# Optimization experiments

Hardware: AMD Instinct MI355X
Metric: run time of the kernel (lower is better)

The kernel has to match this reference:

```python
import jax, jax.numpy as jnp
import numpy as np

N, M = 1024, 32
FN, FE = 64, 32
AGG_N, AGG_E = 128, 64
OUT_N, OUT_E = 64, 32


def _build_indices(n, m):
    nip, eip = [], []
    k = 0
    for i in range(1, n):
        j0 = max(0, i - m)
        nip += list(range(j0, i))
        eip += list(range(k, k + i - j0))
        k += i - j0
    n1 = np.array(nip, np.int32)
    eT = np.array(eip, np.int32)
    n2 = np.concatenate([np.full(min(i, m), i, np.int32) for i in range(1, n)])
    # padded previous-node window indices (0 = zero pad slot)
    prev_nodes = np.zeros(n * m, np.int32)
    k = 0
    for i in range(n):
        t = min(i, m)
        prev_nodes[(i + 1) * m - t:(i + 1) * m] = np.arange(k, k + t) + 1
        k += t
    n_e = k
    norm_node = np.full(n, 1.0 / m, np.float32)
    for i in range(1, m):
        norm_node[i] = 1.0 / i
    prev_edges = np.zeros(n_e * m, np.int32)
    k = 0
    e = 0
    for i in range(n):
        j0 = max(0, i - m)
        for j in range(j0, i):
            if j > j0:
                prev_edges[(e + 1) * m - (j - j0):(e + 1) * m] = np.arange(k, k + j - j0) + 1
            e += 1
        k += i - j0
    norm_edge = np.ones(n_e, np.float32)
    k = 0
    for i in range(1, n):
        t = min(i, m)
        for j in range(t):
            if j > 0:
                norm_edge[k] = 1.0 / j
            k += 1
    return n1, eT, n2, prev_nodes, norm_node, prev_edges, norm_edge, n_e

N1, ET, N2, PREV_N, NORM_N, PREV_E, NORM_E, NE = _build_indices(N, M)
N1 = jnp.asarray(N1); ET = jnp.asarray(ET); N2 = jnp.asarray(N2)
PREV_N = jnp.asarray(PREV_N); PREV_E = jnp.asarray(PREV_E)
NORM_N = jnp.asarray(NORM_N); NORM_E = jnp.asarray(NORM_E)


def setup_inputs() -> dict:
    key = jax.random.key(0)
    ks = jax.random.split(key, 20)
    s = 0.02
    inp = {
        'input_nodes': jax.random.normal(ks[0], (2, N, FN), jnp.float32),
        'input_edges': jax.random.normal(ks[1], (2, NE, FE), jnp.float32),
        # node-branch MLPs (exclude_last=False)
        'Wan1': jax.random.normal(ks[2], (2 * FN + FE, 2 * AGG_N)) * s,
        'ban1': jnp.zeros((2 * AGG_N,)),
        'Wan2': jax.random.normal(ks[3], (2 * AGG_N, AGG_N)) * s,
        'ban2': jnp.zeros((AGG_N,)),
        'Wln1': jax.random.normal(ks[4], (AGG_N + FN, AGG_N + FN)) * s,
        'bln1': jnp.zeros((AGG_N + FN,)),
        'Wln2': jax.random.normal(ks[5], (AGG_N + FN, OUT_N)) * s,
        'bln2': jnp.zeros((OUT_N,)),
        # edge-branch MLPs
        'Wae1': jax.random.normal(ks[6], (FN + FE, 2 * AGG_E)) * s,
        'bae1': jnp.zeros((2 * AGG_E,)),
        'Wae2': jax.random.normal(ks[7], (2 * AGG_E, AGG_E)) * s,
        'bae2': jnp.zeros((AGG_E,)),
        'Wle1': jax.random.normal(ks[8], (AGG_E + FE, AGG_E + FE)) * s,
        'ble1': jnp.zeros((AGG_E + FE,)),
        'Wle2': jax.random.normal(ks[9], (AGG_E + FE, OUT_E)) * s,
        'ble2': jnp.zeros((OUT_E,)),
    }
    return inp


def _mlp2(x, W1, b1, W2, b2):
    return jax.nn.relu(jax.nn.relu(x @ W1 + b1) @ W2 + b2)


def reference(input_nodes, input_edges, Wan1, ban1, Wan2, ban2, Wln1, bln1, Wln2, bln2,
              Wae1, bae1, Wae2, bae2, Wle1, ble1, Wle2, ble2):
    B = input_nodes.shape[0]
    # gather node-edge pairs [B, NE, FN+FE] and node-edge-node triples [B, NE, 2FN+FE]
    pairs = jnp.concatenate([input_nodes[:, N1], input_edges[:, ET]], axis=-1)
    triples = jnp.concatenate([input_nodes[:, N1], input_edges[:, ET], input_nodes[:, N2]], axis=-1)
    # node branch (exclude_last=False -> triples)
    hn = _mlp2(triples, Wan1, ban1, Wan2, ban2)                     # [B, NE, AGG_N]
    hn = jnp.concatenate([jnp.zeros((B, 1, AGG_N), hn.dtype), hn], axis=1)
    pn = hn[:, PREV_N].reshape(B, N, M, AGG_N).sum(axis=2)          # padded window sum
    pn = pn * NORM_N[None, :, None]
    nodes_in = jnp.concatenate([pn, input_nodes], axis=-1)
    out_nodes = _mlp2(nodes_in, Wln1, bln1, Wln2, bln2)             # activation_nodes = relu
    # edge branch (pairs)
    he = _mlp2(pairs, Wae1, bae1, Wae2, bae2)                       # [B, NE, AGG_E]
    he = jnp.concatenate([jnp.zeros((B, 1, AGG_E), he.dtype), he], axis=1)
    pe = he[:, PREV_E].reshape(B, NE, M, AGG_E).sum(axis=2)
    pe = pe * NORM_E[None, :, None]
    edges_in = jnp.concatenate([pe, input_edges], axis=-1)
    out_edges = _mlp2(edges_in, Wle1, ble1, Wle2, ble2)             # activation_edges = relu
    return out_nodes, out_edges
```

## Files before the change

### kernel.cpp

```cpp
#include <hip/hip_runtime.h>
#include <cstdint>

#define NN    1024
#define MM    32
#define NEDGE 32240
#define MROWS 64480
#define PX    168
#define PSTN  264
#define PXE   104
#define PH1   136
#define PHE   72
#define EHALF 9984

typedef unsigned short ushort_t;

typedef __bf16 bf16x8 __attribute__((ext_vector_type(8)));
typedef float  floatx4 __attribute__((ext_vector_type(4)));

__device__ __forceinline__ float b2f(ushort_t u) {
    union { unsigned int i; float f; } v; v.i = ((unsigned int)u) << 16; return v.f;
}
__device__ __forceinline__ ushort_t f2b(float f) {
    return __builtin_bit_cast(ushort_t, (__bf16)f);
}
__device__ __forceinline__ int edge_base(int i) {
    return (i <= MM) ? ((i * (i - 1)) >> 1) : (496 + (i - MM) * MM);
}

__global__ __launch_bounds__(256) void k_pack(
        const float* an1, const float* an2, const float* ae1, const float* ae2,
        const float* le1, const float* le2, const float* ln1, const float* ln2,
        const float* nodes, const float* edges,
        ushort_t* pan1, ushort_t* pan2, ushort_t* pae1, ushort_t* pae2,
        ushort_t* ple1, ushort_t* ple2, ushort_t* pln1, ushort_t* pln2,
        ushort_t* nodesb, ushort_t* edgesb) {
    __shared__ float tile[32][33];
    const int bid = blockIdx.x;
    const int tid = threadIdx.x;
    if (bid < 152) {
        const float* s; ushort_t* d; int K, N, t;
        if (bid < 40)       { s = an1; d = pan1; K = 160; N = 256; t = bid;       }
        else if (bid < 72)  { s = an2; d = pan2; K = 256; N = 128; t = bid - 40;  }
        else if (bid < 84)  { s = ae1; d = pae1; K = 96;  N = 128; t = bid - 72;  }
        else if (bid < 92)  { s = ae2; d = pae2; K = 128; N = 64;  t = bid - 84;  }
        else if (bid < 101) { s = le1; d = ple1; K = 96;  N = 96;  t = bid - 92;  }
        else if (bid < 104) { s = le2; d = ple2; K = 96;  N = 32;  t = bid - 101; }
        else if (bid < 140) { s = ln1; d = pln1; K = 192; N = 192; t = bid - 104; }
        else                { s = ln2; d = pln2; K = 192; N = 64;  t = bid - 140; }
        int ntn = N >> 5;
        int tk = t / ntn, tn = t - tk * ntn;
        int k0 = tk * 32, n0 = tn * 32;
        int tx = tid & 31, ty = tid >> 5;
#pragma unroll
        for (int m = 0; m < 4; ++m)
            tile[ty + m * 8][tx] = s[(size_t)(k0 + ty + m * 8) * N + n0 + tx];
        __syncthreads();
#pragma unroll
        for (int m = 0; m < 4; ++m)
            d[(size_t)(n0 + ty + m * 8) * K + k0 + tx] = f2b(tile[tx][ty + m * 8]);
    } else if (bid < 280) {
        int i4 = (bid - 152) * 256 + tid;
        float4 v = ((const float4*)nodes)[i4];
        uint2 o;
        o.x = (unsigned)f2b(v.x) | ((unsigned)f2b(v.y) << 16);
        o.y = (unsigned)f2b(v.z) | ((unsigned)f2b(v.w) << 16);
        ((uint2*)nodesb)[i4] = o;
    } else {
        int i4 = (bid - 280) * 256 + tid;
        if (i4 < 515840) {
            float4 v = ((const float4*)edges)[i4];
            uint2 o;
            o.x = (unsigned)f2b(v.x) | ((unsigned)f2b(v.y) << 16);
            o.y = (unsigned)f2b(v.z) | ((unsigned)f2b(v.w) << 16);
            ((uint2*)edgesb)[i4] = o;
        }
    }
}

__global__ __launch_bounds__(512, 4) void k_main(
        const ushort_t* __restrict__ nodesb, const ushort_t* __restrict__ edgesb,
        const ushort_t* __restrict__ pan1, const float* __restrict__ ban1,
        const ushort_t* __restrict__ pan2, const float* __restrict__ ban2,
        const ushort_t* __restrict__ pae1, const float* __restrict__ bae1,
        const ushort_t* __restrict__ pae2, const float* __restrict__ bae2,
        const ushort_t* __restrict__ ple1, const float* __restrict__ ble1,
        const ushort_t* __restrict__ ple2, const float* __restrict__ ble2,
        ushort_t* __restrict__ pn, float* __restrict__ out_edges) {
    __shared__ alignas(16) ushort_t SH[2 * EHALF];
    const int tid = threadIdx.x;
    const int w = tid >> 6, l = tid & 63, lrow = l & 15, lq = l >> 4;
    const int bid = blockIdx.x;
    floatx4 zero = {0.f, 0.f, 0.f, 0.f};

    if (bid < 2048) {
        const int b = bid >> 10, i = bid & 1023;
        const int t = min(i, MM);
        if (i == 0) {
            if (tid < 64) ((unsigned*)(pn + (size_t)bid * 128))[tid] = 0u;
            return;
        }
        const int j0 = i - t;
        const int base = b * NEDGE + edge_base(i);
        ushort_t* X = SH;
        ushort_t* H = SH + 32 * PX;

        bf16x8 B0[5], B1[5];
#pragma unroll
        for (int kt = 0; kt < 5; ++kt) {
            B0[kt] = *(const bf16x8*)(pan1 + (size_t)(16 * w + lrow) * 160 + kt * 32 + lq * 8);
            B1[kt] = *(const bf16x8*)(pan1 + (size_t)(16 * (w + 8) + lrow) * 160 + kt * 32 + lq * 8);
        }
        float c0 = ban1[16 * w + lrow];
        float c1 = ban1[16 * (w + 8) + lrow];

#pragma unroll
        for (int k = 0; k < 4; ++k) {
            int rr = w * 4 + k;
            unsigned* xr = (unsigned*)(X + rr * PX);
            const unsigned* nj = (const unsigned*)(nodesb + (size_t)(b * NN + j0 + rr) * 64);
            const unsigned* ni = (const unsigned*)(nodesb + (size_t)(b * NN + i) * 64);
            const unsigned* eb = (const unsigned*)(edgesb + (size_t)(base + rr) * 32);
            if (l < 32) { xr[l] = nj[l]; xr[48 + l] = ni[l]; }
            else        xr[l] = eb[l - 32];
        }
        __syncthreads();

#pragma unroll
        for (int s = 0; s < 2; ++s) {
            bf16x8 A[5];
#pragma unroll
            for (int kt = 0; kt < 5; ++kt)
                A[kt] = *(const bf16x8*)&X[(s * 16 + lrow) * PX + kt * 32 + lq * 8];
            floatx4 a0 = zero, a1 = zero;
#pragma unroll
            for (int kt = 0; kt < 5; ++kt) {
                a0 = __builtin_amdgcn_mfma_f32_16x16x32_bf16(A[kt], B0[kt], a0, 0, 0, 0);
                a1 = __builtin_amdgcn_mfma_f32_16x16x32_bf16(A[kt], B1[kt], a1, 0, 0, 0);
            }
#pragma unroll
            for (int r_ = 0; r_ < 4; ++r_) {
                int row = (s * 16 + lq * 4 + r_) * PSTN;
                H[row + 16 * w + lrow]       = f2b(fmaxf(a0[r_] + c0, 0.f));
                H[row + 128 + 16 * w + lrow] = f2b(fmaxf(a1[r_] + c1, 0.f));
            }
        }
        __syncthreads();

        {
            bf16x8 D[8];
#pragma unroll
            for (int kt = 0; kt < 8; ++kt)
                D[kt] = *(const bf16x8*)(pan2 + (size_t)(16 * w + lrow) * 256 + kt * 32 + lq * 8);
            float d0 = ban2[16 * w + lrow];
            float P = 0.f;
#pragma unroll
            for (int s = 0; s < 2; ++s) {
                floatx4 a0 = zero;
#pragma unroll
                for (int kt = 0; kt < 8; ++kt) {
                    bf16x8 a = *(const bf16x8*)&H[(s * 16 + lrow) * PSTN + kt * 32 + lq * 8];
                    a0 = __builtin_amdgcn_mfma_f32_16x16x32_bf16(a, D[kt], a0, 0, 0, 0);
                }
#pragma unroll
                for (int r_ = 0; r_ < 4; ++r_) {
                    int row = s * 16 + lq * 4 + r_;
                    float v = fmaxf(a0[r_] + d0, 0.f);
                    float vr = b2f(f2b(v));
                    if (row < t) P += vr;
                }
            }
            P += __shfl_xor(P, 16);
            P += __shfl_xor(P, 32);
            if (l < 16)
                pn[(size_t)bid * 128 + 16 * w + lrow] = f2b(P * (1.0f / (float)t));
        }
    } else {
        const int q = bid - 2048;
        const int h = w >> 2, w4 = w & 3;
        const int lt = tid & 255;
        const int ri = 2 * q + h;
        const int b = ri >> 10, i = ri & 1023;
        const int t = min(i, MM);
        const int j0 = i - t;
        const int base = b * NEDGE + edge_base(i);
        ushort_t* Xe = SH + h * EHALF;
        ushort_t* H1 = Xe + 3328;
        ushort_t* HE = H1 + 4352;
        ushort_t* LB = H1;

        bf16x8 B0[3], B1[3];
#pragma unroll
        for (int kt = 0; kt < 3; ++kt) {
            B0[kt] = *(const bf16x8*)(pae1 + (size_t)(16 * w4 + lrow) * 96 + kt * 32 + lq * 8);
            B1[kt] = *(const bf16x8*)(pae1 + (size_t)(16 * (w4 + 4) + lrow) * 96 + kt * 32 + lq * 8);
        }
        const float c0 = bae1[16 * w4 + lrow];
        const float c1 = bae1[16 * (w4 + 4) + lrow];

        for (int u = lt; u < 32 * 48; u += 256) {
            int row = u / 48, c = u - row * 48;
            unsigned v;
            if (c < 32) v = ((const unsigned*)nodesb)[(size_t)(b * NN + j0 + row) * 32 + c];
            else        v = ((const unsigned*)edgesb)[(size_t)(base + row) * 16 + (c - 32)];
            ((unsigned*)Xe)[row * (PXE / 2) + c] = v;
        }
        __syncthreads();

#pragma unroll
        for (int s = 0; s < 2; ++s) {
            bf16x8 A[3];
#pragma unroll
            for (int kt = 0; kt < 3; ++kt)
                A[kt] = *(const bf16x8*)&Xe[(s * 16 + lrow) * PXE + kt * 32 + lq * 8];
            floatx4 a0 = zero, a1 = zero;
#pragma unroll
            for (int kt = 0; kt < 3; ++kt) {
                a0 = __builtin_amdgcn_mfma_f32_16x16x32_bf16(A[kt], B0[kt], a0, 0, 0, 0);
                a1 = __builtin_amdgcn_mfma_f32_16x16x32_bf16(A[kt], B1[kt], a1, 0, 0, 0);
            }
#pragma unroll
            for (int r_ = 0; r_ < 4; ++r_) {
                int row = (s * 16 + lq * 4 + r_) * PH1;
                H1[row + 16 * w4 + lrow]      = f2b(fmaxf(a0[r_] + c0, 0.f));
                H1[row + 64 + 16 * w4 + lrow] = f2b(fmaxf(a1[r_] + c1, 0.f));
            }
        }
        __syncthreads();

        {
            bf16x8 E[4];
#pragma unroll
            for (int kt = 0; kt < 4; ++kt)
                E[kt] = *(const bf16x8*)(pae2 + (size_t)(16 * w4 + lrow) * 128 + kt * 32 + lq * 8);
            float d2 = bae2[16 * w4 + lrow];
#pragma unroll
            for (int s = 0; s < 2; ++s) {
                floatx4 a2 = zero;
#pragma unroll
                for (int kt = 0; kt < 4; ++kt) {
                    bf16x8 a = *(const bf16x8*)&H1[(s * 16 + lrow) * PH1 + kt * 32 + lq * 8];
                    a2 = __builtin_amdgcn_mfma_f32_16x16x32_bf16(a, E[kt], a2, 0, 0, 0);
                }
#pragma unroll
                for (int r_ = 0; r_ < 4; ++r_)
                    HE[(s * 16 + lq * 4 + r_) * PHE + 16 * w4 + lrow] = f2b(fmaxf(a2[r_] + d2, 0.f));
            }
        }
        if (l < 16) {
            float run = 0.f;
            for (int p = 0; p < t; ++p) {
                Xe[p * PXE + 16 * w4 + l] = f2b((p == 0) ? 0.f : run / (float)p);
                run += b2f(HE[p * PHE + 16 * w4 + l]);
            }
        }
        __syncthreads();

        {
            bf16x8 F0[3], F1[3];
            const bool two = (w4 < 2);
#pragma unroll
            for (int kt = 0; kt < 3; ++kt) {
                F0[kt] = *(const bf16x8*)(ple1 + (size_t)(16 * w4 + lrow) * 96 + kt * 32 + lq * 8);
                if (two)
                    F1[kt] = *(const bf16x8*)(ple1 + (size_t)(16 * (w4 + 4) + lrow) * 96 + kt * 32 + lq * 8);
            }
            float v0 = ble1[16 * w4 + lrow];
            float v1 = two ? ble1[16 * (w4 + 4) + lrow] : 0.f;
#pragma unroll
            for (int s = 0; s < 2; ++s) {
                bf16x8 A[3];
#pragma unroll
                for (int kt = 0; kt < 3; ++kt)
                    A[kt] = *(const bf16x8*)&Xe[(s * 16 + lrow) * PXE + kt * 32 + lq * 8];
                floatx4 a0 = zero, a1 = zero;
#pragma unroll
                for (int kt = 0; kt < 3; ++kt) {
                    a0 = __builtin_amdgcn_mfma_f32_16x16x32_bf16(A[kt], F0[kt], a0, 0, 0, 0);
                    if (two)
                        a1 = __builtin_amdgcn_mfma_f32_16x16x32_bf16(A[kt], F1[kt], a1, 0, 0, 0);
                }
#pragma unroll
                for (int r_ = 0; r_ < 4; ++r_) {
                    int row = (s * 16 + lq * 4 + r_) * PXE;
                    LB[row + 16 * w4 + lrow] = f2b(fmaxf(a0[r_] + v0, 0.f));
                    if (two)
                        LB[row + 64 + 16 * w4 + lrow] = f2b(fmaxf(a1[r_] + v1, 0.f));
                }
            }
        }
        __syncthreads();

        {
            int ct = w4 & 1, s = w4 >> 1;
            int c0o = 16 * ct;
            bf16x8 F2[3];
#pragma unroll
            for (int kt = 0; kt < 3; ++kt)
                F2[kt] = *(const bf16x8*)(ple2 + (size_t)(c0o + lrow) * 96 + kt * 32 + lq * 8);
            float v2 = ble2[c0o + lrow];
            floatx4 a2 = zero;
#pragma unroll
            for (int kt = 0; kt < 3; ++kt) {
                bf16x8 a = *(const bf16x8*)&LB[(s * 16 + lrow) * PXE + kt * 32 + lq * 8];
                a2 = __builtin_amdgcn_mfma_f32_16x16x32_bf16(a, F2[kt], a2, 0, 0, 0);
            }
#pragma unroll
            for (int r_ = 0; r_ < 4; ++r_) {
                int grow = s * 16 + lq * 4 + r_;
                if (grow < t)
                    out_edges[(size_t)(base + grow) * 32 + c0o + lrow] = fmaxf(a2[r_] + v2, 0.f);
            }
        }
    }
}

__global__ __launch_bounds__(192) void k_final(
        const ushort_t* __restrict__ pn, const ushort_t* __restrict__ nodesb,
        const ushort_t* __restrict__ pln1, const float* __restrict__ bln1,
        const ushort_t* __restrict__ pln2, const float* __restrict__ bln2,
        float* __restrict__ out_nodes) {
    __shared__ alignas(16) ushort_t LA[32 * 200];
    __shared__ alignas(16) ushort_t LB[32 * 200];
    const int tid = threadIdx.x;
    const int w = tid >> 6, l = tid & 63, lrow = l & 15, lq = l >> 4;
    floatx4 zero = {0.f, 0.f, 0.f, 0.f};

    int tile = blockIdx.x;
    for (int u = tid; u < 768; u += 192) {
        int row = u / 24, c = u - row * 24;
        int r = tile * 32 + row;
        const uint4* src = (c < 16) ? ((const uint4*)(pn + (size_t)r * 128) + c)
                                    : ((const uint4*)(nodesb + (size_t)r * 64) + (c - 16));
        *(uint4*)&LA[row * 200 + c * 8] = *src;
    }
    bf16x8 f1[6][4]; float v1[4];
#pragma unroll
    for (int kt = 0; kt < 6; ++kt)
#pragma unroll
        for (int nt = 0; nt < 4; ++nt)
            f1[kt][nt] = *(const bf16x8*)(pln1 + (size_t)(w * 64 + nt * 16 + lrow) * 192 + kt * 32 + lq * 8);
#pragma unroll
    for (int nt = 0; nt < 4; ++nt) v1[nt] = bln1[w * 64 + nt * 16 + lrow];
    __syncthreads();

    floatx4 acc[2][4];
#pragma unroll
    for (int s = 0; s < 2; ++s)
#pragma unroll
        for (int nt = 0; nt < 4; ++nt) acc[s][nt] = zero;
#pragma unroll
    for (int s = 0; s < 2; ++s)
#pragma unroll
        for (int kt = 0; kt < 6; ++kt) {
            bf16x8 a = *(const bf16x8*)&LA[(s * 16 + lrow) * 200 + kt * 32 + lq * 8];
#pragma unroll
            for (int nt = 0; nt < 4; ++nt)
                acc[s][nt] = __builtin_amdgcn_mfma_f32_16x16x32_bf16(a, f1[kt][nt], acc[s][nt], 0, 0, 0);
        }
#pragma unroll
    for (int s = 0; s < 2; ++s)
#pragma unroll
        for (int nt = 0; nt < 4; ++nt) {
            int col = w * 64 + nt * 16 + lrow;
#pragma unroll
            for (int r_ = 0; r_ < 4; ++r_)
                LB[(s * 16 + lq * 4 + r_) * 200 + col] = f2b(fmaxf(acc[s][nt][r_] + v1[nt], 0.f));
        }
    bf16x8 f2[6][2]; float v2[2] = {0.f, 0.f};
    if (w < 2) {
#pragma unroll
        for (int kt = 0; kt < 6; ++kt)
#pragma unroll
            for (int nt = 0; nt < 2; ++nt)
                f2[kt][nt] = *(const bf16x8*)(pln2 + (size_t)(w * 32 + nt * 16 + lrow) * 192 + kt * 32 + lq * 8);
#pragma unroll
        for (int nt = 0; nt < 2; ++nt) v2[nt] = bln2[w * 32 + nt * 16 + lrow];
    }
    __syncthreads();
    if (w < 2) {
        floatx4 a2[2][2];
#pragma unroll
        for (int s = 0; s < 2; ++s) { a2[s][0] = zero; a2[s][1] = zero; }
#pragma unroll
        for (int s = 0; s < 2; ++s)
#pragma unroll
            for (int kt = 0; kt < 6; ++kt) {
                bf16x8 a = *(const bf16x8*)&LB[(s * 16 + lrow) * 200 + kt * 32 + lq * 8];
#pragma unroll
                for (int nt = 0; nt < 2; ++nt)
                    a2[s][nt] = __builtin_amdgcn_mfma_f32_16x16x32_bf16(a, f2[kt][nt], a2[s][nt], 0, 0, 0);
            }
#pragma unroll
        for (int s = 0; s < 2; ++s)
#pragma unroll
            for (int nt = 0; nt < 2; ++nt) {
                int col = w * 32 + nt * 16 + lrow;
#pragma unroll
                for (int r_ = 0; r_ < 4; ++r_)
                    out_nodes[(size_t)(tile * 32 + s * 16 + lq * 4 + r_) * 64 + col] =
                        fmaxf(a2[s][nt][r_] + v2[nt], 0.f);
            }
    }
}

extern "C" void kernel_launch(void* const* d_in, const int* in_sizes, int n_in,
                              void* d_out, int out_size, void* d_ws, size_t ws_size,
                              hipStream_t stream) {
    const float* nodes = (const float*)d_in[0];
    const float* edges = (const float*)d_in[1];
    const float* Wan1 = (const float*)d_in[2];  const float* ban1 = (const float*)d_in[3];
    const float* Wan2 = (const float*)d_in[4];  const float* ban2 = (const float*)d_in[5];
    const float* Wln1 = (const float*)d_in[6];  const float* bln1 = (const float*)d_in[7];
    const float* Wln2 = (const float*)d_in[8];  const float* bln2 = (const float*)d_in[9];
    const float* Wae1 = (const float*)d_in[10]; const float* bae1 = (const float*)d_in[11];
    const float* Wae2 = (const float*)d_in[12]; const float* bae2 = (const float*)d_in[13];
    const float* Wle1 = (const float*)d_in[14]; const float* ble1 = (const float*)d_in[15];
    const float* Wle2 = (const float*)d_in[16]; const float* ble2 = (const float*)d_in[17];

    char* ws = (char*)d_ws;
    size_t o = 0;
    auto alloc = [&](size_t bytes) -> void* {
        void* r = ws + o;
        o += (bytes + 255) & ~(size_t)255;
        return r;
    };
    ushort_t* pn     = (ushort_t*)alloc((size_t)2048 * 128 * 2);
    ushort_t* nodesb = (ushort_t*)alloc((size_t)2 * NN * 64 * 2);
    ushort_t* edgesb = (ushort_t*)alloc((size_t)MROWS * 32 * 2);
    ushort_t* pan1 = (ushort_t*)alloc(160 * 256 * 2);
    ushort_t* pan2 = (ushort_t*)alloc(256 * 128 * 2);
    ushort_t* pae1 = (ushort_t*)alloc(96 * 128 * 2);
    ushort_t* pae2 = (ushort_t*)alloc(128 * 64 * 2);
    ushort_t* ple1 = (ushort_t*)alloc(96 * 96 * 2);
    ushort_t* ple2 = (ushort_t*)alloc(96 * 32 * 2);
    ushort_t* pln1 = (ushort_t*)alloc(192 * 192 * 2);
    ushort_t* pln2 = (ushort_t*)alloc(192 * 64 * 2);

    float* out_nodes = (float*)d_out;
    float* out_edges = (float*)d_out + 2 * NN * 64;

    k_pack<<<2296, 256, 0, stream>>>(Wan1, Wan2, Wae1, Wae2, Wle1, Wle2, Wln1, Wln2,
                                     nodes, edges,
                                     pan1, pan2, pae1, pae2, ple1, ple2, pln1, pln2,
                                     nodesb, edgesb);
    k_main<<<3072, 512, 0, stream>>>(nodesb, edgesb,
                                     pan1, ban1, pan2, ban2,
                                     pae1, bae1, pae2, bae2,
                                     ple1, ble1, ple2, ble2,
                                     pn, out_edges);
    k_final<<<64, 192, 0, stream>>>(pn, nodesb, pln1, bln1, pln2, bln2, out_nodes);

    (void)in_sizes; (void)n_in; (void)out_size; (void)ws_size;
}
```

Before: 154.9 us.

## Fuse node and edge branches into one block per target node

Merges the separate node-branch and edge-branch blocks so each block handles one target node for both MLP branches. The first-layer GEMM shares the same staged X tile (the edge branch input is a prefix of the triple input), and the second layers run concurrently on different wavefront groups. This removes duplicate gathering of node/edge rows and one-third of the blocks, but raises per-block register and LDS use and puts more serial work in each block, including the single-lane-group scan.

```diff
diff --git a/kernel.cpp b/kernel.cpp
--- a/kernel.cpp
+++ b/kernel.cpp
@@ -6,11 +6,9 @@
 #define NEDGE 32240
 #define MROWS 64480
 #define PX    168
-#define PSTN  264
-#define PXE   104
-#define PH1   136
+#define PST   392
+#define PLB   104
 #define PHE   72
-#define EHALF 9984
 
 typedef unsigned short ushort_t;
 
@@ -86,230 +84,178 @@
         const ushort_t* __restrict__ ple1, const float* __restrict__ ble1,
         const ushort_t* __restrict__ ple2, const float* __restrict__ ble2,
         ushort_t* __restrict__ pn, float* __restrict__ out_edges) {
-    __shared__ alignas(16) ushort_t SH[2 * EHALF];
+    __shared__ alignas(16) ushort_t X[32 * PX];
+    __shared__ alignas(16) ushort_t H[32 * PST];
+    __shared__ alignas(16) ushort_t HE[32 * PHE];
     const int tid = threadIdx.x;
     const int w = tid >> 6, l = tid & 63, lrow = l & 15, lq = l >> 4;
     const int bid = blockIdx.x;
     floatx4 zero = {0.f, 0.f, 0.f, 0.f};
 
-    if (bid < 2048) {
-        const int b = bid >> 10, i = bid & 1023;
-        const int t = min(i, MM);
-        if (i == 0) {
-            if (tid < 64) ((unsigned*)(pn + (size_t)bid * 128))[tid] = 0u;
-            return;
-        }
-        const int j0 = i - t;
-        const int base = b * NEDGE + edge_base(i);
-        ushort_t* X = SH;
-        ushort_t* H = SH + 32 * PX;
-
-        bf16x8 B0[5], B1[5];
+    const int b = bid >> 10, i = bid & 1023;
+    const int t = min(i, MM);
+    if (i == 0) {
+        if (tid < 64) ((unsigned*)(pn + (size_t)bid * 128))[tid] = 0u;
+        return;
+    }
+    const int j0 = i - t;
+    const int base = b * NEDGE + edge_base(i);
+
+    bf16x8 B0[5], B1[5], B2[3];
+#pragma unroll
+    for (int kt = 0; kt < 5; ++kt) {
+        B0[kt] = *(const bf16x8*)(pan1 + (size_t)(16 * w + lrow) * 160 + kt * 32 + lq * 8);
+        B1[kt] = *(const bf16x8*)(pan1 + (size_t)(16 * (w + 8) + lrow) * 160 + kt * 32 + lq * 8);
+    }
+#pragma unroll
+    for (int kt = 0; kt < 3; ++kt)
+        B2[kt] = *(const bf16x8*)(pae1 + (size_t)(16 * w + lrow) * 96 + kt * 32 + lq * 8);
+    const float c0 = ban1[16 * w + lrow];
+    const float c1 = ban1[16 * (w + 8) + lrow];
+    const float c2 = bae1[16 * w + lrow];
+
+#pragma unroll
+    for (int k = 0; k < 4; ++k) {
+        int rr = w * 4 + k;
+        unsigned* xr = (unsigned*)(X + rr * PX);
+        const unsigned* nj = (const unsigned*)(nodesb + (size_t)(b * NN + j0 + rr) * 64);
+        const unsigned* ni = (const unsigned*)(nodesb + (size_t)(b * NN + i) * 64);
+        const unsigned* eb = (const unsigned*)(edgesb + (size_t)(base + rr) * 32);
+        if (l < 32)      { xr[l] = nj[l]; xr[48 + l] = ni[l]; }
+        else if (l < 48)   xr[l] = eb[l - 32];
+    }
+    __syncthreads();
+
+#pragma unroll
+    for (int s = 0; s < 2; ++s) {
+        bf16x8 A[5];
+#pragma unroll
+        for (int kt = 0; kt < 5; ++kt)
+            A[kt] = *(const bf16x8*)&X[(s * 16 + lrow) * PX + kt * 32 + lq * 8];
+        floatx4 a0 = zero, a1 = zero, a2 = zero;
 #pragma unroll
         for (int kt = 0; kt < 5; ++kt) {
-            B0[kt] = *(const bf16x8*)(pan1 + (size_t)(16 * w + lrow) * 160 + kt * 32 + lq * 8);
-            B1[kt] = *(const bf16x8*)(pan1 + (size_t)(16 * (w + 8) + lrow) * 160 + kt * 32 + lq * 8);
-        }
-        float c0 = ban1[16 * w + lrow];
-        float c1 = ban1[16 * (w + 8) + lrow];
-
-#pragma unroll
-        for (int k = 0; k < 4; ++k) {
-            int rr = w * 4 + k;
-            unsigned* xr = (unsigned*)(X + rr * PX);
-            const unsigned* nj = (const unsigned*)(nodesb + (size_t)(b * NN + j0 + rr) * 64);
-            const unsigned* ni = (const unsigned*)(nodesb + (size_t)(b * NN + i) * 64);
-            const unsigned* eb = (const unsigned*)(edgesb + (size_t)(base + rr) * 32);
-            if (l < 32) { xr[l] = nj[l]; xr[48 + l] = ni[l]; }
-            else        xr[l] = eb[l - 32];
-        }
-        __syncthreads();
-
+            a0 = __builtin_amdgcn_mfma_f32_16x16x32_bf16(A[kt], B0[kt], a0, 0, 0, 0);
+            a1 = __builtin_amdgcn_mfma_f32_16x16x32_bf16(A[kt], B1[kt], a1, 0, 0, 0);
+        }
+#pragma unroll
+        for (int kt = 0; kt < 3; ++kt)
+            a2 = __builtin_amdgcn_mfma_f32_16x16x32_bf16(A[kt], B2[kt], a2, 0, 0, 0);
+#pragma unroll
+        for (int r_ = 0; r_ < 4; ++r_) {
+            int row = (s * 16 + lq * 4 + r_) * PST;
+            H[row + 16 * w + lrow]       = f2b(fmaxf(a0[r_] + c0, 0.f));
+            H[row + 128 + 16 * w + lrow] = f2b(fmaxf(a1[r_] + c1, 0.f));
+            H[row + 256 + 16 * w + lrow] = f2b(fmaxf(a2[r_] + c2, 0.f));
+        }
+    }
+    __syncthreads();
+
+    if (w < 4) {
+        bf16x8 D0[8], D1[8];
+#pragma unroll
+        for (int kt = 0; kt < 8; ++kt) {
+            D0[kt] = *(const bf16x8*)(pan2 + (size_t)(16 * w + lrow) * 256 + kt * 32 + lq * 8);
+            D1[kt] = *(const bf16x8*)(pan2 + (size_t)(16 * (w + 4) + lrow) * 256 + kt * 32 + lq * 8);
+        }
+        float d0 = ban2[16 * w + lrow];
+        float d1 = ban2[16 * (w + 4) + lrow];
+        float P0 = 0.f, P1 = 0.f;
 #pragma unroll
         for (int s = 0; s < 2; ++s) {
-            bf16x8 A[5];
-#pragma unroll
-            for (int kt = 0; kt < 5; ++kt)
-                A[kt] = *(const bf16x8*)&X[(s * 16 + lrow) * PX + kt * 32 + lq * 8];
             floatx4 a0 = zero, a1 = zero;
 #pragma unroll
-            for (int kt = 0; kt < 5; ++kt) {
-                a0 = __builtin_amdgcn_mfma_f32_16x16x32_bf16(A[kt], B0[kt], a0, 0, 0, 0);
-                a1 = __builtin_amdgcn_mfma_f32_16x16x32_bf16(A[kt], B1[kt], a1, 0, 0, 0);
+            for (int kt = 0; kt < 8; ++kt) {
+                bf16x8 a = *(const bf16x8*)&H[(s * 16 + lrow) * PST + kt * 32 + lq * 8];
+                a0 = __builtin_amdgcn_mfma_f32_16x16x32_bf16(a, D0[kt], a0, 0, 0, 0);
+                a1 = __builtin_amdgcn_mfma_f32_16x16x32_bf16(a, D1[kt], a1, 0, 0, 0);
             }
 #pragma unroll
             for (int r_ = 0; r_ < 4; ++r_) {
-                int row = (s * 16 + lq * 4 + r_) * PSTN;
-                H[row + 16 * w + lrow]       = f2b(fmaxf(a0[r_] + c0, 0.f));
-                H[row + 128 + 16 * w + lrow] = f2b(fmaxf(a1[r_] + c1, 0.f));
-            }
-        }
-        __syncthreads();
-
-        {
-            bf16x8 D[8];
-#pragma unroll
-            for (int kt = 0; kt < 8; ++kt)
-                D[kt] = *(const bf16x8*)(pan2 + (size_t)(16 * w + lrow) * 256 + kt * 32 + lq * 8);
-            float d0 = ban2[16 * w + lrow];
-            float P = 0.f;
-#pragma unroll
-            for (int s = 0; s < 2; ++s) {
-                floatx4 a0 = zero;
-#pragma unroll
-                for (int kt = 0; kt < 8; ++kt) {
-                    bf16x8 a = *(const bf16x8*)&H[(s * 16 + lrow) * PSTN + kt * 32 + lq * 8];
-                    a0 = __builtin_amdgcn_mfma_f32_16x16x32_bf16(a, D[kt], a0, 0, 0, 0);
-                }
-#pragma unroll
-                for (int r_ = 0; r_ < 4; ++r_) {
-                    int row = s * 16 + lq * 4 + r_;
-                    float v = fmaxf(a0[r_] + d0, 0.f);
-                    float vr = b2f(f2b(v));
-                    if (row < t) P += vr;
-                }
-            }
-            P += __shfl_xor(P, 16);
-            P += __shfl_xor(P, 32);
-            if (l < 16)
-                pn[(size_t)bid * 128 + 16 * w + lrow] = f2b(P * (1.0f / (float)t));
+                int row = s * 16 + lq * 4 + r_;
+                float v0 = b2f(f2b(fmaxf(a0[r_] + d0, 0.f)));
+                float v1 = b2f(f2b(fmaxf(a1[r_] + d1, 0.f)));
+                if (row < t) { P0 += v0; P1 += v1; }
+            }
+        }
+        P0 += __shfl_xor(P0, 16); P0 += __shfl_xor(P0, 32);
+        P1 += __shfl_xor(P1, 16); P1 += __shfl_xor(P1, 32);
+        if (l < 16) {
+            float inv = 1.0f / (float)t;
+            pn[(size_t)bid * 128 + 16 * w + lrow]       = f2b(P0 * inv);
+            pn[(size_t)bid * 128 + 16 * (w + 4) + lrow] = f2b(P1 * inv);
         }
     } else {
-        const int q = bid - 2048;
-        const int h = w >> 2, w4 = w & 3;
-        const int lt = tid & 255;
-        const int ri = 2 * q + h;
-        const int b = ri >> 10, i = ri & 1023;
-        const int t = min(i, MM);
-        const int j0 = i - t;
-        const int base = b * NEDGE + edge_base(i);
-        ushort_t* Xe = SH + h * EHALF;
-        ushort_t* H1 = Xe + 3328;
-        ushort_t* HE = H1 + 4352;
-        ushort_t* LB = H1;
-
-        bf16x8 B0[3], B1[3];
-#pragma unroll
-        for (int kt = 0; kt < 3; ++kt) {
-            B0[kt] = *(const bf16x8*)(pae1 + (size_t)(16 * w4 + lrow) * 96 + kt * 32 + lq * 8);
-            B1[kt] = *(const bf16x8*)(pae1 + (size_t)(16 * (w4 + 4) + lrow) * 96 + kt * 32 + lq * 8);
-        }
-        const float c0 = bae1[16 * w4 + lrow];
-        const float c1 = bae1[16 * (w4 + 4) + lrow];
-
-        for (int u = lt; u < 32 * 48; u += 256) {
-            int row = u / 48, c = u - row * 48;
-            unsigned v;
-            if (c < 32) v = ((const unsigned*)nodesb)[(size_t)(b * NN + j0 + row) * 32 + c];
-            else        v = ((const unsigned*)edgesb)[(size_t)(base + row) * 16 + (c - 32)];
-            ((unsigned*)Xe)[row * (PXE / 2) + c] = v;
-        }
-        __syncthreads();
-
+        int u = w - 4;
+        bf16x8 E[4];
+#pragma unroll
+        for (int kt = 0; kt < 4; ++kt)
+            E[kt] = *(const bf16x8*)(pae2 + (size_t)(16 * u + lrow) * 128 + kt * 32 + lq * 8);
+        float d2 = bae2[16 * u + lrow];
 #pragma unroll
         for (int s = 0; s < 2; ++s) {
-            bf16x8 A[3];
-#pragma unroll
-            for (int kt = 0; kt < 3; ++kt)
-                A[kt] = *(const bf16x8*)&Xe[(s * 16 + lrow) * PXE + kt * 32 + lq * 8];
-            floatx4 a0 = zero, a1 = zero;
-#pragma unroll
-            for (int kt = 0; kt < 3; ++kt) {
-                a0 = __builtin_amdgcn_mfma_f32_16x16x32_bf16(A[kt], B0[kt], a0, 0, 0, 0);
-                a1 = __builtin_amdgcn_mfma_f32_16x16x32_bf16(A[kt], B1[kt], a1, 0, 0, 0);
-            }
-#pragma unroll
-            for (int r_ = 0; r_ < 4; ++r_) {
-                int row = (s * 16 + lq * 4 + r_) * PH1;
-                H1[row + 16 * w4 + lrow]      = f2b(fmaxf(a0[r_] + c0, 0.f));
-                H1[row + 64 + 16 * w4 + lrow] = f2b(fmaxf(a1[r_] + c1, 0.f));
-            }
-        }
-        __syncthreads();
-
-        {
-            bf16x8 E[4];
-#pragma unroll
-            for (int kt = 0; kt < 4; ++kt)
-                E[kt] = *(const bf16x8*)(pae2 + (size_t)(16 * w4 + lrow) * 128 + kt * 32 + lq * 8);
-            float d2 = bae2[16 * w4 + lrow];
-#pragma unroll
-            for (int s = 0; s < 2; ++s) {
-                floatx4 a2 = zero;
-#pragma unroll
-                for (int kt = 0; kt < 4; ++kt) {
-                    bf16x8 a = *(const bf16x8*)&H1[(s * 16 + lrow) * PH1 + kt * 32 + lq * 8];
-                    a2 = __builtin_amdgcn_mfma_f32_16x16x32_bf16(a, E[kt], a2, 0, 0, 0);
-                }
-#pragma unroll
-                for (int r_ = 0; r_ < 4; ++r_)
-                    HE[(s * 16 + lq * 4 + r_) * PHE + 16 * w4 + lrow] = f2b(fmaxf(a2[r_] + d2, 0.f));
-            }
+            floatx4 a2 = zero;
+#pragma unroll
+            for (int kt = 0; kt < 4; ++kt) {
+                bf16x8 a = *(const bf16x8*)&H[(s * 16 + lrow) * PST + 256 + kt * 32 + lq * 8];
+                a2 = __builtin_amdgcn_mfma_f32_16x16x32_bf16(a, E[kt], a2, 0, 0, 0);
+            }
+#pragma unroll
+            for (int r_ = 0; r_ < 4; ++r_)
+                HE[(s * 16 + lq * 4 + r_) * PHE + 16 * u + lrow] = f2b(fmaxf(a2[r_] + d2, 0.f));
         }
         if (l < 16) {
             float run = 0.f;
             for (int p = 0; p < t; ++p) {
-                Xe[p * PXE + 16 * w4 + l] = f2b((p == 0) ? 0.f : run / (float)p);
-                run += b2f(HE[p * PHE + 16 * w4 + l]);
-            }
-        }
-        __syncthreads();
-
-        {
-            bf16x8 F0[3], F1[3];
-            const bool two = (w4 < 2);
-#pragma unroll
-            for (int kt = 0; kt < 3; ++kt) {
-                F0[kt] = *(const bf16x8*)(ple1 + (size_t)(16 * w4 + lrow) * 96 + kt * 32 + lq * 8);
-                if (two)
-                    F1[kt] = *(const bf16x8*)(ple1 + (size_t)(16 * (w4 + 4) + lrow) * 96 + kt * 32 + lq * 8);
-            }
-            float v0 = ble1[16 * w4 + lrow];
-            float v1 = two ? ble1[16 * (w4 + 4) + lrow] : 0.f;
-#pragma unroll
-            for (int s = 0; s < 2; ++s) {
-                bf16x8 A[3];
-#pragma unroll
-                for (int kt = 0; kt < 3; ++kt)
-                    A[kt] = *(const bf16x8*)&Xe[(s * 16 + lrow) * PXE + kt * 32 + lq * 8];
-                floatx4 a0 = zero, a1 = zero;
-#pragma unroll
-                for (int kt = 0; kt < 3; ++kt) {
-                    a0 = __builtin_amdgcn_mfma_f32_16x16x32_bf16(A[kt], F0[kt], a0, 0, 0, 0);
-                    if (two)
-                        a1 = __builtin_amdgcn_mfma_f32_16x16x32_bf16(A[kt], F1[kt], a1, 0, 0, 0);
-                }
-#pragma unroll
-                for (int r_ = 0; r_ < 4; ++r_) {
-                    int row = (s * 16 + lq * 4 + r_) * PXE;
-                    LB[row + 16 * w4 + lrow] = f2b(fmaxf(a0[r_] + v0, 0.f));
-                    if (two)
-                        LB[row + 64 + 16 * w4 + lrow] = f2b(fmaxf(a1[r_] + v1, 0.f));
-                }
-            }
-        }
-        __syncthreads();
-
-        {
-            int ct = w4 & 1, s = w4 >> 1;
-            int c0o = 16 * ct;
-            bf16x8 F2[3];
+                X[p * PX + 16 * u + l] = f2b((p == 0) ? 0.f : run / (float)p);
+                run += b2f(HE[p * PHE + 16 * u + l]);
+            }
+        }
+    }
+    __syncthreads();
+
+    if (w < 6) {
+        bf16x8 F0[3];
+#pragma unroll
+        for (int kt = 0; kt < 3; ++kt)
+            F0[kt] = *(const bf16x8*)(ple1 + (size_t)(16 * w + lrow) * 96 + kt * 32 + lq * 8);
+        float v0 = ble1[16 * w + lrow];
+#pragma unroll
+        for (int s = 0; s < 2; ++s) {
+            bf16x8 A[3];
 #pragma unroll
             for (int kt = 0; kt < 3; ++kt)
-                F2[kt] = *(const bf16x8*)(ple2 + (size_t)(c0o + lrow) * 96 + kt * 32 + lq * 8);
-            float v2 = ble2[c0o + lrow];
-            floatx4 a2 = zero;
-#pragma unroll
-            for (int kt = 0; kt < 3; ++kt) {
-                bf16x8 a = *(const bf16x8*)&LB[(s * 16 + lrow) * PXE + kt * 32 + lq * 8];
-                a2 = __builtin_amdgcn_mfma_f32_16x16x32_bf16(a, F2[kt], a2, 0, 0, 0);
-            }
-#pragma unroll
-            for (int r_ = 0; r_ < 4; ++r_) {
-                int grow = s * 16 + lq * 4 + r_;
-                if (grow < t)
-                    out_edges[(size_t)(base + grow) * 32 + c0o + lrow] = fmaxf(a2[r_] + v2, 0.f);
-            }
+                A[kt] = *(const bf16x8*)&X[(s * 16 + lrow) * PX + kt * 32 + lq * 8];
+            floatx4 a0 = zero;
+#pragma unroll
+            for (int kt = 0; kt < 3; ++kt)
+                a0 = __builtin_amdgcn_mfma_f32_16x16x32_bf16(A[kt], F0[kt], a0, 0, 0, 0);
+#pragma unroll
+            for (int r_ = 0; r_ < 4; ++r_)
+                H[(s * 16 + lq * 4 + r_) * PLB + 16 * w + lrow] = f2b(fmaxf(a0[r_] + v0, 0.f));
+        }
+    }
+    __syncthreads();
+
+    if (w < 4) {
+        int ct = w & 1, s2 = w >> 1;
+        int c0o = 16 * ct;
+        bf16x8 F2[3];
+#pragma unroll
+        for (int kt = 0; kt < 3; ++kt)
+            F2[kt] = *(const bf16x8*)(ple2 + (size_t)(c0o + lrow) * 96 + kt * 32 + lq * 8);
+        float v2 = ble2[c0o + lrow];
+        floatx4 a2 = zero;
+#pragma unroll
+        for (int kt = 0; kt < 3; ++kt) {
+            bf16x8 a = *(const bf16x8*)&H[(s2 * 16 + lrow) * PLB + kt * 32 + lq * 8];
+            a2 = __builtin_amdgcn_mfma_f32_16x16x32_bf16(a, F2[kt], a2, 0, 0, 0);
+        }
+#pragma unroll
+        for (int r_ = 0; r_ < 4; ++r_) {
+            int grow = s2 * 16 + lq * 4 + r_;
+            if (grow < t)
+                out_edges[(size_t)(base + grow) * 32 + c0o + lrow] = fmaxf(a2[r_] + v2, 0.f);
         }
     }
 }
@@ -443,7 +389,7 @@
                                      nodes, edges,
                                      pan1, pan2, pae1, pae2, ple1, ple2, pln1, pln2,
                                      nodesb, edgesb);
-    k_main<<<3072, 512, 0, stream>>>(nodesb, edgesb,
+    k_main<<<2048, 512, 0, stream>>>(nodesb, edgesb,
                                      pan1, ban1, pan2, ban2,
                                      pae1, bae1, pae2, bae2,
                                      ple1, ble1, ple2, ble2,
```

Result: no change. 156.5 us (+1.1%).
